# Kernel tuning notes

Measured on AMD Instinct MI355X. Metric: run time of the kernel, lower is better.

## Reference

```python
import jax, jax.numpy as jnp
import numpy as np

# Model config (matches init_kwargs)
DATA_L = 256
LATENT_L = 64
LATENT_N = 8
N_COMPS = 8
LOG_2PI = float(np.log(2.0 * np.pi))


def setup_inputs() -> dict:
    key = jax.random.key(0)
    ks = jax.random.split(key, 7)
    B = 2048
    N = B * LATENT_N  # 16384
    x = jax.random.normal(ks[0], (B, DATA_L), dtype=jnp.float32)
    W_e = jax.random.normal(ks[1], (DATA_L, LATENT_L * N_COMPS * 3), dtype=jnp.float32) * 0.05
    b_e = jnp.zeros((LATENT_L * N_COMPS * 3,), dtype=jnp.float32)
    W_d = jax.random.normal(ks[2], (LATENT_L, DATA_L * N_COMPS * 3), dtype=jnp.float32) * 0.05
    b_d = jnp.zeros((DATA_L * N_COMPS * 3,), dtype=jnp.float32)
    u_e = jax.random.normal(ks[3], (N, LATENT_L), dtype=jnp.float32)
    r = jax.random.uniform(ks[4], (N, LATENT_L), dtype=jnp.float32)
    return {"x": x, "W_e": W_e, "b_e": b_e, "W_d": W_d, "b_d": b_d, "u_e": u_e, "r": r}


def _split3(pred, K, D):
    # pred: (N, 3*K*D) -> m, logp, loga each (N, K, D)
    m = pred[:, : K * D].reshape(-1, K, D)
    logp = pred[:, K * D : 2 * K * D].reshape(-1, K, D)
    loga = pred[:, 2 * K * D :].reshape(-1, K, D)
    loga = jax.nn.log_softmax(loga, axis=1)  # loga - logsumexp over comps
    return m, logp, loga


def _discrete_sample(loga, r):
    # loga: (N, K, D), r: (N, D). Matches torch: idx = sum((r > cumsum(p)).int(), dim=1)
    c = jnp.cumsum(jnp.exp(loga), axis=1)  # (N, K, D)
    idx = jnp.sum((r[:, None, :] > c).astype(jnp.int32), axis=1)  # (N, D)
    return jnp.clip(idx, 0, loga.shape[1] - 1)


def reference(x, W_e, b_e, W_d, b_d, u_e, r):
    K, L, D = N_COMPS, LATENT_L, DATA_L
    x_rep = jnp.tile(x, (LATENT_N, 1))  # (N, D)

    # Encoder (KAN with width=[data_l, 3*K*L] modeled as dense layer)
    pred_e = x_rep @ W_e + b_e  # (N, 3*K*L)
    m_e, logp_e, loga_e = _split3(pred_e, K, L)

    # Sample mixture component per (row, latent dim), gather, reparameterize
    idx = _discrete_sample(loga_e, r)  # (N, L) int32
    m_sel = jnp.take_along_axis(m_e, idx[:, None, :], axis=1)[:, 0, :]  # (N, L)
    logp_sel = jnp.take_along_axis(logp_e, idx[:, None, :], axis=1)[:, 0, :]
    h = m_sel + jnp.exp(-0.5 * logp_sel) * u_e  # (N, L)

    # log q(h|x): mixture-of-Gaussians density at h
    uh = jnp.exp(0.5 * logp_e) * (h[:, None, :] - m_e)  # (N, K, L)
    L_e = jax.nn.logsumexp(loga_e - 0.5 * uh * uh + 0.5 * logp_e, axis=1)  # (N, L)
    L_e = -0.5 * L * LOG_2PI + jnp.sum(L_e, axis=1)  # (N,)

    # log prior N(0, I)
    L_q = -0.5 * L * LOG_2PI - 0.5 * jnp.sum(h * h, axis=1)  # (N,)

    # Decoder mixture likelihood of x
    pred_d = h @ W_d + b_d  # (N, 3*K*D)
    m_d, logp_d, loga_d = _split3(pred_d, K, D)
    ux = jnp.exp(0.5 * logp_d) * (x_rep[:, None, :] - m_d)  # (N, K, D)
    L_d = jax.nn.logsumexp(loga_d - 0.5 * ux * ux + 0.5 * logp_d, axis=1)  # (N, D)
    L_d = -0.5 * D * LOG_2PI + jnp.sum(L_d, axis=1)  # (N,)

    return -jnp.mean(L_d + L_q - L_e)
```

## Files before the change

kernel.cpp:

```cpp
#include <hip/hip_runtime.h>
#include <hip/hip_bf16.h>
#include <math.h>

#define D_L   256
#define L_L   64
#define K_C   8
#define BATCH 2048
#define NTOT  16384
#define ENC_COLS 1536
#define LOG2PI 1.8378770664093453f
#define L2E    1.4426950408889634f
#define LN2    0.6931471805599453f
#define C_HL2E 0.7213475204444817f

typedef __attribute__((ext_vector_type(8)))  short short8;
typedef __attribute__((ext_vector_type(8)))  unsigned short ushort8;
typedef __attribute__((ext_vector_type(4)))  unsigned short ushort4_;
typedef __attribute__((ext_vector_type(4)))  float float4_;
typedef __attribute__((ext_vector_type(16))) float float16_;

#if defined(__has_builtin)
#  if __has_builtin(__builtin_amdgcn_exp2f)
#    define EXP2F(x) __builtin_amdgcn_exp2f(x)
#  endif
#  if __has_builtin(__builtin_amdgcn_logf)
#    define LOG2F(x) __builtin_amdgcn_logf(x)
#  endif
#endif
#ifndef EXP2F
#  define EXP2F(x) __expf((x) * LN2)
#endif
#ifndef LOG2F
#  define LOG2F(x) (__logf(x) * L2E)
#endif

#define OFF_PE    0
#define OFF_H     (BATCH * ENC_COLS)
#define OFF_WET2  (OFF_H + NTOT * L_L / 2)
#define OFF_WDT2  (OFF_WET2 + ENC_COLS * D_L / 2)
#define OFF_ACC   (OFF_WDT2 + 6144 * 64 / 2)
#define OFF_CNT   (OFF_ACC + 1)

__device__ __forceinline__ unsigned short f2bf(float f) {
  unsigned u = __float_as_uint(f);
  return (unsigned short)((u + 0x7fffu + ((u >> 16) & 1u)) >> 16);
}

__global__ __launch_bounds__(256) void k_prep(
    const float* __restrict__ We, const float* __restrict__ Wd,
    unsigned short* __restrict__ WeT2, unsigned short* __restrict__ WdT2,
    float* __restrict__ accf, unsigned* __restrict__ counter)
{
  const int bid = blockIdx.x, t = threadIdx.x;
  if (bid == 192) {
    if (t == 0) { accf[0] = 0.0f; counter[0] = 0u; }
    return;
  }

  const float* src; int C, rowbase, colbase; float scale;
  unsigned short* dst;
  if (bid < 96) {
    const int comp = bid / 12, p = (bid % 12) >> 2, dt = bid & 3;
    src = Wd; C = 6144; rowbase = 0;
    colbase = p * 2048 + comp * 256 + dt * 64;
    scale = p ? L2E : 1.0f;
    dst = WdT2 + (size_t)bid * 4096;
  } else {
    const int idx = bid - 96;
    src = We; C = ENC_COLS; rowbase = (idx & 3) * 64;
    colbase = (idx >> 2) * 64;
    scale = 1.0f;
    dst = WeT2 + (size_t)idx * 4096;
  }

  __shared__ float tile[64][65];
  {
    const int col = t & 63, w0 = t >> 6;
    #pragma unroll
    for (int i = 0; i < 16; ++i) {
      const int r = w0 + i * 4;
      tile[r][col] = src[(size_t)(rowbase + r) * C + colbase + col] * scale;
    }
  }
  __syncthreads();
  const int st = t >> 6, q = (t >> 5) & 1, c = t & 31;
  #pragma unroll
  for (int dg = 0; dg < 2; ++dg) {
    ushort8 o;
    #pragma unroll
    for (int j = 0; j < 8; ++j) o[j] = f2bf(tile[st * 16 + q * 8 + j][dg * 32 + c]);
    *(ushort8*)(dst + ((((size_t)dg * 4 + st) * 2 + q) * 32 + c) * 8) = o;
  }
}

__global__ __launch_bounds__(256) void k_enc(
    const float* __restrict__ x, const unsigned short* __restrict__ WeT2,
    const float* __restrict__ be, float* __restrict__ pe)
{
  __shared__ __align__(16) unsigned short as_[64 * 264];
  const int t = threadIdx.x;
  const int w = t >> 6, l = t & 63;
  const int col = l & 31, q = l >> 5;
  const int rg = w >> 1, dg = w & 1;
  const int m0 = blockIdx.y * 64, cblk = blockIdx.x, c0 = cblk * 64;

  {
    const int kc4 = (t & 63) * 4;
    #pragma unroll
    for (int i = 0; i < 16; ++i) {
      const int r = (t >> 6) + i * 4;
      float4_ v = *(const float4_*)(x + (size_t)(m0 + r) * D_L + kc4);
      ushort4_ o;
      o[0] = f2bf(v[0]); o[1] = f2bf(v[1]); o[2] = f2bf(v[2]); o[3] = f2bf(v[3]);
      *(ushort4_*)&as_[r * 264 + kc4] = o;
    }
  }

  const float bias = be[c0 + dg * 32 + col];
  float16_ acc;
  #pragma unroll
  for (int e = 0; e < 16; ++e) acc[e] = bias;

  __syncthreads();

  const unsigned short* arow = &as_[(rg * 32 + col) * 264 + q * 8];
  const unsigned short* bbase = WeT2 + (size_t)cblk * 16384 + dg * 2048 + l * 8;
  #pragma unroll
  for (int kc = 0; kc < 4; ++kc) {
    #pragma unroll
    for (int st = 0; st < 4; ++st) {
      short8 a = *(const short8*)(arow + kc * 64 + st * 16);
      short8 b = *(const short8*)(bbase + (size_t)kc * 4096 + st * 512);
      acc = __builtin_amdgcn_mfma_f32_32x32x16_bf16(a, b, acc, 0, 0, 0);
    }
  }
  #pragma unroll
  for (int e = 0; e < 16; ++e) {
    const int row = (e & 3) + 8 * (e >> 2) + 4 * q;
    pe[(size_t)(m0 + rg * 32 + row) * ENC_COLS + c0 + dg * 32 + col] = acc[e];
  }
}

__global__ __launch_bounds__(256) void k_enc_post(
    const float* __restrict__ pe, const float* __restrict__ ue,
    const float* __restrict__ rr, unsigned short* __restrict__ h,
    float* __restrict__ accf)
{
  const int lane = threadIdx.x & 63;
  const int w = threadIdx.x >> 6;
  const int b = blockIdx.x * 4 + w;
  const float* row = pe + (size_t)b * ENC_COLS + lane;

  float m[8], p[8], a[8];
  #pragma unroll
  for (int k = 0; k < K_C; ++k) {
    m[k] = row[k * 64]; p[k] = row[512 + k * 64]; a[k] = row[1024 + k * 64];
  }
  float amax = a[0];
  #pragma unroll
  for (int k = 1; k < K_C; ++k) amax = fmaxf(amax, a[k]);
  float sa = 0.f;
  #pragma unroll
  for (int k = 0; k < K_C; ++k) sa += __expf(a[k] - amax);
  const float lse_a = amax + __logf(sa);

  float cum[8];
  {
    float cs = 0.f;
    #pragma unroll
    for (int k = 0; k < K_C; ++k) { cs += __expf(a[k] - lse_a); cum[k] = cs; }
  }
  float ep[8];
  #pragma unroll
  for (int k = 0; k < K_C; ++k) ep[k] = __expf(p[k]);

  const int st = lane >> 4, qq = (lane >> 3) & 1, jj = lane & 7;

  float tot = 0.f;
  for (int j = 0; j < 8; ++j) {
    const int n = b + BATCH * j;
    const float rv = rr[(size_t)n * L_L + lane];
    const float uv = ue[(size_t)n * L_L + lane];
    int idx = 0;
    #pragma unroll
    for (int k = 0; k < K_C; ++k) idx += (rv > cum[k]) ? 1 : 0;
    idx = min(idx, K_C - 1);
    float msel = m[0], psel = p[0];
    #pragma unroll
    for (int k = 1; k < K_C; ++k) {
      const bool sel = (idx == k);
      msel = sel ? m[k] : msel;
      psel = sel ? p[k] : psel;
    }
    const float hv = fmaf(__expf(-0.5f * psel), uv, msel);

    const int nblk = n >> 6, rgn = (n >> 5) & 1, coln = n & 31;
    h[((((size_t)(nblk * 2 + rgn) * 4 + st) * 2 + qq) * 32 + coln) * 8 + jj] = f2bf(hv);

    float stt = 0.f;
    #pragma unroll
    for (int k = 0; k < K_C; ++k) {
      const float dd = hv - m[k];
      const float tt = a[k] + 0.5f * p[k] - 0.5f * ep[k] * dd * dd;
      stt += __expf(tt);
    }
    tot += -0.5f * hv * hv - (__logf(stt + 1e-30f) - lse_a);
  }
  #pragma unroll
  for (int off = 1; off < 64; off <<= 1) tot += __shfl_xor(tot, off, 64);
  __shared__ float red2[4];
  if (lane == 0) red2[w] = tot;
  __syncthreads();
  if (threadIdx.x == 0) atomicAdd(accf, red2[0] + red2[1] + red2[2] + red2[3]);
}

__global__ __launch_bounds__(256, 2) void k_dec(
    const unsigned short* __restrict__ hF, const float* __restrict__ x,
    const unsigned short* __restrict__ WdT2, const float* __restrict__ bd,
    float* __restrict__ accf, unsigned* __restrict__ counter,
    float* __restrict__ out)
{
  const int t = threadIdx.x;
  const int w = t >> 6, l = t & 63;
  const int col = l & 31, q = l >> 5;
  const int rg = w >> 1, dg = w & 1;
  const int dt = blockIdx.x, d0 = dt * 64;
  const int nblk = blockIdx.y, n0 = nblk * 64;
  const int colD = d0 + dg * 32 + col;

  const unsigned short* hbase = hF + ((size_t)(nblk * 2 + rg) * 4) * 512 + l * 8;
  short8 af[4];
  #pragma unroll
  for (int st = 0; st < 4; ++st) af[st] = *(const short8*)(hbase + st * 512);

  float bmv[8], bpv[8], bav[8];
  #pragma unroll
  for (int c = 0; c < K_C; ++c) {
    bmv[c] = bd[c * 256 + colD];
    bpv[c] = bd[2048 + c * 256 + colD] * L2E;
    bav[c] = bd[4096 + c * 256 + colD] * L2E;
  }

  float xv[16];
  #pragma unroll
  for (int e = 0; e < 16; ++e) {
    const int rw = (e & 3) + 8 * (e >> 2) + 4 * q;
    const int n = n0 + rg * 32 + rw;
    xv[e] = x[(size_t)(n & (BATCH - 1)) * D_L + colD];
  }

  float s_a[16], s_t[16];
  #pragma unroll
  for (int e = 0; e < 16; ++e) { s_a[e] = 0.f; s_t[e] = 0.f; }

  const unsigned short* wbase = WdT2 + dg * 2048 + l * 8;

  short8 bA[3][4], bB[3][4];

#define LOADB(BUF, comp)                                                     \
  {                                                                          \
    _Pragma("unroll")                                                        \
    for (int p = 0; p < 3; ++p) {                                            \
      const unsigned short* pb =                                             \
          wbase + ((size_t)((comp) * 3 + p) * 4 + dt) * 4096;                \
      _Pragma("unroll")                                                      \
      for (int st = 0; st < 4; ++st)                                         \
        BUF[p][st] = *(const short8*)(pb + st * 512);                        \
    }                                                                        \
  }

#define COMPB(BUF, comp)                                                     \
  {                                                                          \
    float16_ am = {}, ap = {}, aa = {};                                      \
    _Pragma("unroll")                                                        \
    for (int st = 0; st < 4; ++st) {                                         \
      am = __builtin_amdgcn_mfma_f32_32x32x16_bf16(af[st], BUF[0][st], am, 0, 0, 0); \
      ap = __builtin_amdgcn_mfma_f32_32x32x16_bf16(af[st], BUF[1][st], ap, 0, 0, 0); \
      aa = __builtin_amdgcn_mfma_f32_32x32x16_bf16(af[st], BUF[2][st], aa, 0, 0, 0); \
    }                                                                        \
    const float bm = bmv[(comp)], bpL = bpv[(comp)], baL = bav[(comp)];      \
    _Pragma("unroll")                                                        \
    for (int e = 0; e < 16; ++e) {                                           \
      const float dd  = xv[e] - (am[e] + bm);                                \
      const float lpL = ap[e] + bpL;                                         \
      const float laL = aa[e] + baL;                                         \
      const float ex2 = EXP2F(lpL);                                          \
      const float t1  = fmaf(0.5f, lpL, laL);                                \
      const float ttL = fmaf(-C_HL2E * ex2, dd * dd, t1);                    \
      s_a[e] += EXP2F(laL);                                                  \
      s_t[e] += EXP2F(ttL);                                                  \
    }                                                                        \
  }

  LOADB(bA, 0)
  LOADB(bB, 1)  COMPB(bA, 0)
  LOADB(bA, 2)  COMPB(bB, 1)
  LOADB(bB, 3)  COMPB(bA, 2)
  LOADB(bA, 4)  COMPB(bB, 3)
  LOADB(bB, 5)  COMPB(bA, 4)
  LOADB(bA, 6)  COMPB(bB, 5)
  LOADB(bB, 7)  COMPB(bA, 6)
                COMPB(bB, 7)

#undef LOADB
#undef COMPB

  float v = 0.f;
  #pragma unroll
  for (int e = 0; e < 16; ++e)
    v += LOG2F(s_t[e] + 1e-30f) - LOG2F(s_a[e]);
  v *= LN2;
  #pragma unroll
  for (int off = 1; off < 64; off <<= 1) v += __shfl_xor(v, off, 64);
  __shared__ float red[4];
  if (l == 0) red[w] = v;
  __syncthreads();
  if (t == 0) {
    atomicAdd(accf, red[0] + red[1] + red[2] + red[3]);
    __threadfence();
    const unsigned c = atomicAdd(counter, 1u);
    if (c == 1023u) {
      __threadfence();
      const float tot = __hip_atomic_load(accf, __ATOMIC_ACQUIRE,
                                          __HIP_MEMORY_SCOPE_AGENT);
      out[0] = -(tot / (float)NTOT) + 128.0f * LOG2PI;
    }
  }
}

extern "C" void kernel_launch(void* const* d_in, const int* in_sizes, int n_in,
                              void* d_out, int out_size, void* d_ws, size_t ws_size,
                              hipStream_t stream)
{
  const float* x  = (const float*)d_in[0];
  const float* We = (const float*)d_in[1];
  const float* be = (const float*)d_in[2];
  const float* Wd = (const float*)d_in[3];
  const float* bd = (const float*)d_in[4];
  const float* ue = (const float*)d_in[5];
  const float* rr = (const float*)d_in[6];
  float* out = (float*)d_out;

  float* ws = (float*)d_ws;
  float* pe            = ws + OFF_PE;
  unsigned short* h    = (unsigned short*)(ws + OFF_H);
  unsigned short* WeT2 = (unsigned short*)(ws + OFF_WET2);
  unsigned short* WdT2 = (unsigned short*)(ws + OFF_WDT2);
  float* accf          = ws + OFF_ACC;
  unsigned* counter    = (unsigned*)(ws + OFF_CNT);

  k_prep<<<dim3(193), 256, 0, stream>>>(We, Wd, WeT2, WdT2, accf, counter);
  k_enc<<<dim3(ENC_COLS / 64, BATCH / 64), 256, 0, stream>>>(x, WeT2, be, pe);
  k_enc_post<<<dim3(BATCH / 4), 256, 0, stream>>>(pe, ue, rr, h, accf);
  k_dec<<<dim3(4, NTOT / 64), 256, 0, stream>>>(h, x, WdT2, bd, accf, counter, out);
}
```

Before: 134.2 us.

## Process two row tiles per wave in decoder to reuse weight fragments

The decoder kernel now handles 128 rows per block instead of 64, so each wave computes two 32-row MFMA tiles against the same loaded W_d fragments. This halves weight traffic per output and halves the grid size. The bias is folded into the accumulator initialisation instead of being added in the epilogue. The double-buffered B registers become a single buffer, with the next component's load issued between the two tiles' MFMA and epilogue phases to overlap latency. The risks are higher register pressure from doubled accumulators and x values, and fewer blocks to fill the GPU.

```diff
diff --git a/kernel.cpp b/kernel.cpp
--- a/kernel.cpp
+++ b/kernel.cpp
@@ -225,90 +225,101 @@
   const int col = l & 31, q = l >> 5;
   const int rg = w >> 1, dg = w & 1;
   const int dt = blockIdx.x, d0 = dt * 64;
-  const int nblk = blockIdx.y, n0 = nblk * 64;
+  const int by = blockIdx.y;
   const int colD = d0 + dg * 32 + col;
 
-  const unsigned short* hbase = hF + ((size_t)(nblk * 2 + rg) * 4) * 512 + l * 8;
-  short8 af[4];
-  #pragma unroll
-  for (int st = 0; st < 4; ++st) af[st] = *(const short8*)(hbase + st * 512);
-
-  float bmv[8], bpv[8], bav[8];
-  #pragma unroll
-  for (int c = 0; c < K_C; ++c) {
-    bmv[c] = bd[c * 256 + colD];
-    bpv[c] = bd[2048 + c * 256 + colD] * L2E;
-    bav[c] = bd[4096 + c * 256 + colD] * L2E;
-  }
-
-  float xv[16];
-  #pragma unroll
-  for (int e = 0; e < 16; ++e) {
-    const int rw = (e & 3) + 8 * (e >> 2) + 4 * q;
-    const int n = n0 + rg * 32 + rw;
-    xv[e] = x[(size_t)(n & (BATCH - 1)) * D_L + colD];
-  }
-
-  float s_a[16], s_t[16];
-  #pragma unroll
-  for (int e = 0; e < 16; ++e) { s_a[e] = 0.f; s_t[e] = 0.f; }
+  short8 af[2][4];
+  #pragma unroll
+  for (int t2 = 0; t2 < 2; ++t2)
+    #pragma unroll
+    for (int st = 0; st < 4; ++st)
+      af[t2][st] = *(const short8*)(hF +
+          ((size_t)(by * 4 + rg * 2 + t2)) * 2048 + st * 512 + l * 8);
+
+  float xv[2][16];
+  #pragma unroll
+  for (int t2 = 0; t2 < 2; ++t2)
+    #pragma unroll
+    for (int e = 0; e < 16; ++e) {
+      const int rw = (e & 3) + 8 * (e >> 2) + 4 * q;
+      const int n = by * 128 + rg * 64 + t2 * 32 + rw;
+      xv[t2][e] = x[(size_t)(n & (BATCH - 1)) * D_L + colD];
+    }
+
+  float s_a[2][16], s_t[2][16];
+  #pragma unroll
+  for (int t2 = 0; t2 < 2; ++t2)
+    #pragma unroll
+    for (int e = 0; e < 16; ++e) { s_a[t2][e] = 0.f; s_t[t2][e] = 0.f; }
 
   const unsigned short* wbase = WdT2 + dg * 2048 + l * 8;
 
-  short8 bA[3][4], bB[3][4];
-
-#define LOADB(BUF, comp)                                                     \
+  short8 bf[3][4];
+  float bmS, bpS, baS;
+  float16_ am, ap, aa;
+
+#define LOADB(comp)                                                          \
   {                                                                          \
+    bmS = bd[(comp) * 256 + colD];                                           \
+    bpS = bd[2048 + (comp) * 256 + colD] * L2E;                              \
+    baS = bd[4096 + (comp) * 256 + colD] * L2E;                              \
     _Pragma("unroll")                                                        \
     for (int p = 0; p < 3; ++p) {                                            \
       const unsigned short* pb =                                             \
           wbase + ((size_t)((comp) * 3 + p) * 4 + dt) * 4096;                \
       _Pragma("unroll")                                                      \
       for (int st = 0; st < 4; ++st)                                         \
-        BUF[p][st] = *(const short8*)(pb + st * 512);                        \
+        bf[p][st] = *(const short8*)(pb + st * 512);                         \
     }                                                                        \
   }
 
-#define COMPB(BUF, comp)                                                     \
+#define MFMAT(T2)                                                            \
   {                                                                          \
-    float16_ am = {}, ap = {}, aa = {};                                      \
+    _Pragma("unroll")                                                        \
+    for (int e = 0; e < 16; ++e) { am[e] = bmS; ap[e] = bpS; aa[e] = baS; }  \
     _Pragma("unroll")                                                        \
     for (int st = 0; st < 4; ++st) {                                         \
-      am = __builtin_amdgcn_mfma_f32_32x32x16_bf16(af[st], BUF[0][st], am, 0, 0, 0); \
-      ap = __builtin_amdgcn_mfma_f32_32x32x16_bf16(af[st], BUF[1][st], ap, 0, 0, 0); \
-      aa = __builtin_amdgcn_mfma_f32_32x32x16_bf16(af[st], BUF[2][st], aa, 0, 0, 0); \
+      am = __builtin_amdgcn_mfma_f32_32x32x16_bf16(af[T2][st], bf[0][st], am, 0, 0, 0); \
+      ap = __builtin_amdgcn_mfma_f32_32x32x16_bf16(af[T2][st], bf[1][st], ap, 0, 0, 0); \
+      aa = __builtin_amdgcn_mfma_f32_32x32x16_bf16(af[T2][st], bf[2][st], aa, 0, 0, 0); \
     }                                                                        \
-    const float bm = bmv[(comp)], bpL = bpv[(comp)], baL = bav[(comp)];      \
+  }
+
+#define EPIT(T2)                                                             \
+  {                                                                          \
     _Pragma("unroll")                                                        \
     for (int e = 0; e < 16; ++e) {                                           \
-      const float dd  = xv[e] - (am[e] + bm);                                \
-      const float lpL = ap[e] + bpL;                                         \
-      const float laL = aa[e] + baL;                                         \
+      const float dd  = xv[T2][e] - am[e];                                   \
+      const float lpL = ap[e];                                               \
+      const float laL = aa[e];                                               \
       const float ex2 = EXP2F(lpL);                                          \
       const float t1  = fmaf(0.5f, lpL, laL);                                \
       const float ttL = fmaf(-C_HL2E * ex2, dd * dd, t1);                    \
-      s_a[e] += EXP2F(laL);                                                  \
-      s_t[e] += EXP2F(ttL);                                                  \
+      s_a[T2][e] += EXP2F(laL);                                              \
+      s_t[T2][e] += EXP2F(ttL);                                              \
     }                                                                        \
   }
 
-  LOADB(bA, 0)
-  LOADB(bB, 1)  COMPB(bA, 0)
-  LOADB(bA, 2)  COMPB(bB, 1)
-  LOADB(bB, 3)  COMPB(bA, 2)
-  LOADB(bA, 4)  COMPB(bB, 3)
-  LOADB(bB, 5)  COMPB(bA, 4)
-  LOADB(bA, 6)  COMPB(bB, 5)
-  LOADB(bB, 7)  COMPB(bA, 6)
-                COMPB(bB, 7)
+  LOADB(0)
+  MFMAT(0) EPIT(0) MFMAT(1) LOADB(1) EPIT(1)
+  MFMAT(0) EPIT(0) MFMAT(1) LOADB(2) EPIT(1)
+  MFMAT(0) EPIT(0) MFMAT(1) LOADB(3) EPIT(1)
+  MFMAT(0) EPIT(0) MFMAT(1) LOADB(4) EPIT(1)
+  MFMAT(0) EPIT(0) MFMAT(1) LOADB(5) EPIT(1)
+  MFMAT(0) EPIT(0) MFMAT(1) LOADB(6) EPIT(1)
+  MFMAT(0) EPIT(0) MFMAT(1) LOADB(7) EPIT(1)
+  MFMAT(0) EPIT(0) MFMAT(1)          EPIT(1)
 
 #undef LOADB
-#undef COMPB
+#undef MFMAT
+#undef EPIT
 
   float v = 0.f;
   #pragma unroll
-  for (int e = 0; e < 16; ++e)
-    v += LOG2F(s_t[e] + 1e-30f) - LOG2F(s_a[e]);
+  for (int t2 = 0; t2 < 2; ++t2)
+    #pragma unroll
+    for (int e = 0; e < 16; ++e)
+      v += LOG2F(s_t[t2][e] + 1e-30f) - LOG2F(s_a[t2][e]);
   v *= LN2;
   #pragma unroll
   for (int off = 1; off < 64; off <<= 1) v += __shfl_xor(v, off, 64);
@@ -319,7 +330,7 @@
     atomicAdd(accf, red[0] + red[1] + red[2] + red[3]);
     __threadfence();
     const unsigned c = atomicAdd(counter, 1u);
-    if (c == 1023u) {
+    if (c == 511u) {
       __threadfence();
       const float tot = __hip_atomic_load(accf, __ATOMIC_ACQUIRE,
                                           __HIP_MEMORY_SCOPE_AGENT);
@@ -352,5 +363,5 @@
   k_prep<<<dim3(193), 256, 0, stream>>>(We, Wd, WeT2, WdT2, accf, counter);
   k_enc<<<dim3(ENC_COLS / 64, BATCH / 64), 256, 0, stream>>>(x, WeT2, be, pe);
   k_enc_post<<<dim3(BATCH / 4), 256, 0, stream>>>(pe, ue, rr, h, accf);
-  k_dec<<<dim3(4, NTOT / 64), 256, 0, stream>>>(h, x, WdT2, bd, accf, counter, out);
-}
+  k_dec<<<dim3(4, NTOT / 128), 256, 0, stream>>>(h, x, WdT2, bd, accf, counter, out);
+}
```

Result: slower. 231.6 us (+72.6%).
